# Kernel tuning notes

Measured on AMD Instinct MI355X. Metric: run time of the kernel, lower is better.

The kernel has to match this reference:

```python
import jax, jax.numpy as jnp
import numpy as np

NEG_SLOPE = 0.2  # both GATConv internal LeakyReLU and the module-level activation


def gat_conv(x, src, dst, W, a_src, a_dst, bias):
    """PyG GATConv (concat=True, add_self_loops handled by caller via src/dst).
    x: [N, Din]; W: [Din, H*C]; a_src, a_dst: [H, C]; bias: [H*C]."""
    N = x.shape[0]
    H, C = a_src.shape
    h = (x @ W).reshape(N, H, C)                       # [N, H, C]
    al_src = jnp.einsum('nhc,hc->nh', h, a_src)        # [N, H]
    al_dst = jnp.einsum('nhc,hc->nh', h, a_dst)        # [N, H]
    e = jax.nn.leaky_relu(al_src[src] + al_dst[dst], NEG_SLOPE)  # [E, H]
    # segment softmax over edges grouped by destination node
    m = jax.ops.segment_max(e, dst, num_segments=N)    # [N, H]
    ex = jnp.exp(e - m[dst])
    denom = jax.ops.segment_sum(ex, dst, num_segments=N)
    alpha = ex / denom[dst]                            # [E, H]
    out = jax.ops.segment_sum(alpha[:, :, None] * h[src], dst, num_segments=N)
    return out.reshape(N, H * C) + bias


def setup_inputs() -> dict:
    key = jax.random.key(0)
    N, E = 50000, 800000
    D_IN, HID, H = 128, 128, 2
    C = HID // H
    ks = jax.random.split(key, 20)
    inp = {
        'x': jax.random.normal(ks[0], (N, D_IN), dtype=jnp.float32),
        'edge_index': jax.random.randint(ks[1], (2, E), 0, N, dtype=jnp.int64),
    }
    dims = [D_IN, HID, HID]  # input dims of the 3 GATConv layers
    for i, din in enumerate(dims, start=1):
        s = 1.0 / np.sqrt(din)
        inp[f'W{i}'] = jax.random.normal(ks[2 + 4 * i], (din, HID), dtype=jnp.float32) * s
        inp[f'a_src{i}'] = jax.random.normal(ks[3 + 4 * i], (H, C), dtype=jnp.float32) * 0.1
        inp[f'a_dst{i}'] = jax.random.normal(ks[4 + 4 * i], (H, C), dtype=jnp.float32) * 0.1
        inp[f'b{i}'] = jnp.zeros((HID,), dtype=jnp.float32)
    inp['lin_w'] = jax.random.normal(ks[2], (HID, 1), dtype=jnp.float32) * (1.0 / np.sqrt(HID))
    inp['lin_b'] = jnp.zeros((1,), dtype=jnp.float32)
    return inp


def reference(x, edge_index, W1, a_src1, a_dst1, b1, W2, a_src2, a_dst2, b2,
              W3, a_src3, a_dst3, b3, lin_w, lin_b):
    N = x.shape[0]
    loops = jnp.arange(N, dtype=edge_index.dtype)
    src = jnp.concatenate([edge_index[0], loops])  # add_self_loops=True
    dst = jnp.concatenate([edge_index[1], loops])

    h = jax.nn.leaky_relu(gat_conv(x, src, dst, W1, a_src1, a_dst1, b1), NEG_SLOPE)
    # dropout is identity in eval mode (p=0.0)
    h = jax.nn.leaky_relu(h + gat_conv(h, src, dst, W2, a_src2, a_dst2, b2), NEG_SLOPE)
    h = jax.nn.leaky_relu(h + gat_conv(h, src, dst, W3, a_src3, a_dst3, b3), NEG_SLOPE)
    logits = (h @ lin_w + lin_b).squeeze(-1)  # [N]
    return logits
```

## Files before the change

kernel.cpp:

```cpp
#include <hip/hip_runtime.h>
#include <hip/hip_bf16.h>
#include <hip/hip_fp16.h>

#define LEAK 0.2f

typedef _Float16 half8  __attribute__((ext_vector_type(8)));
typedef _Float16 half4v __attribute__((ext_vector_type(4)));
typedef float    float4v __attribute__((ext_vector_type(4)));


__global__ __launch_bounds__(256) void k_bincount(const int* __restrict__ edst,
                                                  int* __restrict__ gbkt,
                                                  int E, int ETOT, int NBK) {
    __shared__ int lh[512];
    int t = threadIdx.x;
    for (int b = t; b < NBK; b += 256) lh[b] = 0;
    __syncthreads();
    int base = blockIdx.x * 4096;
    #pragma unroll
    for (int u = 0; u < 16; ++u) {
        int e = base + u * 256 + t;
        if (e < ETOT) {
            int d = (e < E) ? edst[e] : (e - E);
            atomicAdd(&lh[d >> 7], 1);
        }
    }
    __syncthreads();
    for (int b = t; b < NBK; b += 256)
        if (lh[b]) atomicAdd(&gbkt[b], lh[b]);
}

__global__ __launch_bounds__(512) void k_bktscan(const int* __restrict__ gbkt,
                                                 int* __restrict__ bko,
                                                 int* __restrict__ gcur, int NBK) {
    int t = threadIdx.x;
    int v = (t < NBK) ? gbkt[t] : 0;
    int lane = t & 63, wid = t >> 6;
    int x = v;
    #pragma unroll
    for (int o = 1; o < 64; o <<= 1) {
        int y = __shfl_up(x, o);
        if (lane >= o) x += y;
    }
    __shared__ int ws[8];
    if (lane == 63) ws[wid] = x;
    __syncthreads();
    if (wid == 0) {
        int s = (lane < 8) ? ws[lane] : 0;
        #pragma unroll
        for (int o = 1; o < 8; o <<= 1) {
            int y = __shfl_up(s, o);
            if (lane >= o) s += y;
        }
        if (lane < 8) ws[lane] = s;
    }
    __syncthreads();
    int excl = x - v + (wid > 0 ? ws[wid - 1] : 0);
    if (t < NBK) { bko[t] = excl; gcur[t] = excl; }
    if (t == 511) bko[NBK] = excl;
}

__global__ __launch_bounds__(256) void k_binscatter(const int* __restrict__ esrc,
                                                    const int* __restrict__ edst,
                                                    int* __restrict__ gcur,
                                                    unsigned int* __restrict__ binned,
                                                    int E, int ETOT, int NBK) {
    __shared__ int lh[512];
    __shared__ int lbase[512];
    int t = threadIdx.x;
    for (int b = t; b < NBK; b += 256) lh[b] = 0;
    __syncthreads();
    int base = blockIdx.x * 4096;
    unsigned int word[16]; int bb[16], rk[16];
    #pragma unroll
    for (int u = 0; u < 16; ++u) {
        int e = base + u * 256 + t;
        bb[u] = -1;
        if (e < ETOT) {
            int s, d;
            if (e < E) { s = esrc[e]; d = edst[e]; } else { s = d = e - E; }
            int b = d >> 7;
            bb[u] = b;
            rk[u] = atomicAdd(&lh[b], 1);
            word[u] = (unsigned int)s | ((unsigned int)(d & 127) << 17);
        }
    }
    __syncthreads();
    for (int b = t; b < NBK; b += 256) {
        int c = lh[b];
        lbase[b] = c ? atomicAdd(&gcur[b], c) : 0;
    }
    __syncthreads();
    #pragma unroll
    for (int u = 0; u < 16; ++u)
        if (bb[u] >= 0) binned[lbase[bb[u]] + rk[u]] = word[u];
}

__global__ __launch_bounds__(256) void k_scatter2(const unsigned int* __restrict__ binned,
                                                  const int* __restrict__ bko,
                                                  int* __restrict__ off,
                                                  int* __restrict__ csr, int N, int NBK) {
    __shared__ int deg[128];
    __shared__ int lcur[128];
    __shared__ int wt[2];
    int b = blockIdx.x, t = threadIdx.x;
    int n0 = b << 7;
    if (t < 128) deg[t] = 0;
    __syncthreads();
    int beg = bko[b], end = bko[b + 1];
    for (int i = beg + t; i < end; i += 256)
        atomicAdd(&deg[binned[i] >> 17], 1);
    __syncthreads();
    int v = 0, x = 0;
    if (t < 128) {
        v = deg[t];
        x = v;
        int lane = t & 63;
        #pragma unroll
        for (int o = 1; o < 64; o <<= 1) {
            int y = __shfl_up(x, o);
            if (lane >= o) x += y;
        }
        if (lane == 63) wt[t >> 6] = x;
    }
    __syncthreads();
    if (t < 128) {
        int excl = x - v + ((t >= 64) ? wt[0] : 0) + beg;
        lcur[t] = excl;
        int node = n0 + t;
        if (node < N) off[node] = excl;
    }
    if (b == NBK - 1 && t == 0) off[N] = end;
    __syncthreads();
    for (int i = beg + t; i < end; i += 256) {
        unsigned int u = binned[i];
        int pos = atomicAdd(&lcur[u >> 17], 1);
        csr[pos] = (int)(u & 0x1FFFF);
    }
}


__global__ __launch_bounds__(256) void k_wconv(const float* __restrict__ W0,
                                               const float* __restrict__ W1,
                                               const float* __restrict__ W2,
                                               _Float16* __restrict__ w16) {
    int i = blockIdx.x * 256 + threadIdx.x;
    if (i >= 3 * 16384) return;
    const float* src = (i < 16384) ? W0 : (i < 32768 ? W1 : W2);
    w16[i] = (_Float16)src[i & 16383];
}


__global__ __launch_bounds__(256) void k_gemm_mfma(const float* __restrict__ X,
                                                   const _Float16* __restrict__ Wh,
                                                   const float* __restrict__ a_src,
                                                   const float* __restrict__ a_dst,
                                                   __half* __restrict__ Hout,
                                                   float* __restrict__ alsrc,
                                                   float* __restrict__ aldst, int N) {
    __shared__ _Float16 As[64][136];
    __shared__ float sS[64][2];
    __shared__ float sD[64][2];
    const int t = threadIdx.x;
    const int lane = t & 63, w = t >> 6;
    const int block_row = blockIdx.x * 64;

    if (t < 128) { sS[t >> 1][t & 1] = 0.f; sD[t >> 1][t & 1] = 0.f; }

    #pragma unroll
    for (int it = 0; it < 8; ++it) {
        int i = t + 256 * it;
        int row = i >> 5, c4 = i & 31;
        int gr = block_row + row;
        float4 xv = make_float4(0.f, 0.f, 0.f, 0.f);
        if (gr < N) xv = *(const float4*)(X + (size_t)gr * 128 + c4 * 4);
        half4v hv;
        hv[0] = (_Float16)xv.x; hv[1] = (_Float16)xv.y;
        hv[2] = (_Float16)xv.z; hv[3] = (_Float16)xv.w;
        *(half4v*)(&As[row][c4 * 4]) = hv;
    }

    const int l15 = lane & 15, kq = (lane >> 4) * 8;
    half8 bf[2][4];
    #pragma unroll
    for (int ntl = 0; ntl < 2; ++ntl) {
        int n0 = (w * 2 + ntl) * 16 + l15;
        #pragma unroll
        for (int kt = 0; kt < 4; ++kt)
            #pragma unroll
            for (int j = 0; j < 8; ++j)
                bf[ntl][kt][j] = Wh[(kt * 32 + kq + j) * 128 + n0];
    }
    __syncthreads();

    float4v acc[4][2];
    #pragma unroll
    for (int mt = 0; mt < 4; ++mt)
        #pragma unroll
        for (int ntl = 0; ntl < 2; ++ntl)
            acc[mt][ntl] = (float4v){0.f, 0.f, 0.f, 0.f};

    #pragma unroll
    for (int kt = 0; kt < 4; ++kt) {
        half8 a[4];
        #pragma unroll
        for (int mt = 0; mt < 4; ++mt)
            a[mt] = *(const half8*)(&As[mt * 16 + l15][kt * 32 + kq]);
        #pragma unroll
        for (int mt = 0; mt < 4; ++mt)
            #pragma unroll
            for (int ntl = 0; ntl < 2; ++ntl)
                acc[mt][ntl] = __builtin_amdgcn_mfma_f32_16x16x32_f16(
                    a[mt], bf[ntl][kt], acc[mt][ntl], 0, 0, 0);
    }

    #pragma unroll
    for (int mt = 0; mt < 4; ++mt) {
        int r0 = block_row + mt * 16 + (lane >> 4) * 4;
        #pragma unroll
        for (int ntl = 0; ntl < 2; ++ntl) {
            int col = (w * 2 + ntl) * 16 + l15;
            #pragma unroll
            for (int reg = 0; reg < 4; ++reg) {
                int r = r0 + reg;
                if (r < N) Hout[(size_t)r * 128 + col] = __float2half((float)acc[mt][ntl][reg]);
            }
        }
    }

    {
        int c0 = w * 32 + l15, c1 = c0 + 16;
        float as0 = a_src[c0], as1 = a_src[c1];
        float ad0 = a_dst[c0], ad1 = a_dst[c1];
        int head = w >> 1;
        #pragma unroll
        for (int mt = 0; mt < 4; ++mt) {
            #pragma unroll
            for (int reg = 0; reg < 4; ++reg) {
                float ps = (float)acc[mt][0][reg] * as0 + (float)acc[mt][1][reg] * as1;
                float pd = (float)acc[mt][0][reg] * ad0 + (float)acc[mt][1][reg] * ad1;
                #pragma unroll
                for (int o = 1; o < 16; o <<= 1) {
                    ps += __shfl_xor(ps, o);
                    pd += __shfl_xor(pd, o);
                }
                if (l15 == 0) {
                    int row = mt * 16 + (lane >> 4) * 4 + reg;
                    atomicAdd(&sS[row][head], ps);
                    atomicAdd(&sD[row][head], pd);
                }
            }
        }
    }
    __syncthreads();
    if (t < 128) {
        int row = t >> 1, head = t & 1;
        int gr = block_row + row;
        if (gr < N) {
            alsrc[gr * 2 + head] = sS[row][head];
            aldst[gr * 2 + head] = sD[row][head];
        }
    }
}


__global__ __launch_bounds__(256) void k_aggregate(
        const __half* __restrict__ H16,
        const float* __restrict__ alsrc,
        const float* __restrict__ aldst,
        const int* __restrict__ off, const int* __restrict__ csr,
        const float* __restrict__ bias,
        const float* __restrict__ prev,
        float* __restrict__ Out,
        const float* __restrict__ lw, const float* __restrict__ lb,
        float* __restrict__ logits, int N, int mode) {
    int node = (int)((blockIdx.x * 256 + threadIdx.x) >> 6);
    int lane = threadIdx.x & 63;
    if (node >= N) return;
    int beg = off[node], end = off[node + 1];
    float ad0 = aldst[node * 2], ad1 = aldst[node * 2 + 1];

    int p = lane & 7;
    int q = lane >> 3;
    bool head0 = p < 4;
    const _Float16* hbase = (const _Float16*)H16 + p * 16;

    float acc[16];
    #pragma unroll
    for (int i = 0; i < 16; ++i) acc[i] = 0.f;
    float dsum = 0.f;

    for (int base = beg; base < end; base += 64) {
        int i = base + lane;
        float w0 = 0.f, w1 = 0.f; int s = 0;
        if (i < end) {
            s = csr[i];
            float2 al = *(const float2*)(&alsrc[s * 2]);
            float e0 = al.x + ad0; e0 = e0 > 0.f ? e0 : LEAK * e0;
            float e1 = al.y + ad1; e1 = e1 > 0.f ? e1 : LEAK * e1;
            w0 = __expf(e0); w1 = __expf(e1);
        }
        int cnt = min(64, end - base);
        int iters = (cnt + 7) >> 3;
        for (int jj = 0; jj < iters; ++jj) {
            int sl = (jj << 3) + q;
            int   sj  = __shfl(s,  sl);
            float w0j = __shfl(w0, sl);
            float w1j = __shfl(w1, sl);
            float wsel = head0 ? w0j : w1j;
            const _Float16* hp = hbase + (size_t)sj * 128;
            uint4 r0 = *(const uint4*)hp;
            uint4 r1 = *(const uint4*)(hp + 8);
            const _Float16* ha = (const _Float16*)&r0;
            const _Float16* hb = (const _Float16*)&r1;
            #pragma unroll
            for (int k = 0; k < 8; ++k) acc[k]     += wsel * (float)ha[k];
            #pragma unroll
            for (int k = 0; k < 8; ++k) acc[8 + k] += wsel * (float)hb[k];
            dsum += wsel;
        }
    }

    #pragma unroll
    for (int i = 0; i < 16; ++i) {
        acc[i] += __shfl_xor(acc[i], 8);
        acc[i] += __shfl_xor(acc[i], 16);
        acc[i] += __shfl_xor(acc[i], 32);
    }
    dsum += __shfl_xor(dsum, 8);
    dsum += __shfl_xor(dsum, 16);
    dsum += __shfl_xor(dsum, 32);

    if (q == 0) {
        float inv = 1.f / dsum;
        int c0 = p * 16;
        float v[16];
        #pragma unroll
        for (int i = 0; i < 16; ++i) v[i] = acc[i] * inv + bias[c0 + i];
        if (mode >= 1) {
            #pragma unroll
            for (int g = 0; g < 4; ++g) {
                float4 pv = *(const float4*)(&prev[(size_t)node * 128 + c0 + 4 * g]);
                v[4 * g]     += pv.x; v[4 * g + 1] += pv.y;
                v[4 * g + 2] += pv.z; v[4 * g + 3] += pv.w;
            }
        }
        #pragma unroll
        for (int i = 0; i < 16; ++i) v[i] = v[i] > 0.f ? v[i] : LEAK * v[i];
        if (mode == 2) {
            float partial = 0.f;
            #pragma unroll
            for (int i = 0; i < 16; ++i) partial += v[i] * lw[c0 + i];
            partial += __shfl_xor(partial, 1);
            partial += __shfl_xor(partial, 2);
            partial += __shfl_xor(partial, 4);
            if (p == 0) logits[node] = partial + lb[0];
        } else {
            #pragma unroll
            for (int g = 0; g < 4; ++g)
                *(float4*)(&Out[(size_t)node * 128 + c0 + 4 * g]) =
                    make_float4(v[4 * g], v[4 * g + 1], v[4 * g + 2], v[4 * g + 3]);
        }
    }
}


extern "C" void kernel_launch(void* const* d_in, const int* in_sizes, int n_in,
                              void* d_out, int out_size, void* d_ws, size_t ws_size,
                              hipStream_t stream) {
    const float* x    = (const float*)d_in[0];
    const int*   edge = (const int*)d_in[1];
    const float* W[3]  = {(const float*)d_in[2], (const float*)d_in[6], (const float*)d_in[10]};
    const float* as[3] = {(const float*)d_in[3], (const float*)d_in[7], (const float*)d_in[11]};
    const float* ad[3] = {(const float*)d_in[4], (const float*)d_in[8], (const float*)d_in[12]};
    const float* bs[3] = {(const float*)d_in[5], (const float*)d_in[9], (const float*)d_in[13]};
    const float* lw = (const float*)d_in[14];
    const float* lb = (const float*)d_in[15];

    const int N    = in_sizes[0] / 128;
    const int E    = in_sizes[1] / 2;
    const int ETOT = E + N;
    const int NBK  = (N + 127) >> 7;

    char* base = (char*)d_ws;
    size_t o = 0;
    auto carve = [&](size_t bytes) {
        char* p = base + o;
        o = (o + bytes + 255) & ~(size_t)255;
        return p;
    };
    int*      off    = (int*)     carve((size_t)(N + 1) * 4);
    int*      gbkt   = (int*)     carve((size_t)(NBK + 1) * 4);
    int*      bko    = (int*)     carve((size_t)(NBK + 1) * 4);
    int*      gcur   = (int*)     carve((size_t)(NBK + 1) * 4);
    unsigned* binned = (unsigned*)carve((size_t)ETOT * 4);
    int*      csr    = (int*)     carve((size_t)ETOT * 4);
    float*    alsrc  = (float*)   carve((size_t)N * 2 * 4);
    float*    aldst  = (float*)   carve((size_t)N * 2 * 4);
    __half*   h16    = (__half*)  carve((size_t)N * 128 * 2);
    float*    bufA   = (float*)   carve((size_t)N * 128 * 4);
    float*    bufB   = (float*)   carve((size_t)N * 128 * 4);
    _Float16* w16    = (_Float16*)carve((size_t)3 * 16384 * 2);
    (void)ws_size; (void)n_in; (void)out_size;

    const int* esrc = edge;
    const int* edst = edge + E;

    int eb = (ETOT + 4095) / 4096;

    hipMemsetAsync(gbkt, 0, (size_t)(NBK + 1) * 4, stream);
    k_wconv<<<192, 256, 0, stream>>>(W[0], W[1], W[2], w16);

    k_bincount<<<eb, 256, 0, stream>>>(edst, gbkt, E, ETOT, NBK);
    k_bktscan<<<1, 512, 0, stream>>>(gbkt, bko, gcur, NBK);
    k_binscatter<<<eb, 256, 0, stream>>>(esrc, edst, gcur, binned, E, ETOT, NBK);
    k_scatter2<<<NBK, 256, 0, stream>>>(binned, bko, off, csr, N, NBK);

    int gemm_blocks = (N + 63) / 64;
    int node_blocks = (N * 64 + 255) / 256;

    k_gemm_mfma<<<gemm_blocks, 256, 0, stream>>>(x, w16, as[0], ad[0], h16, alsrc, aldst, N);
    k_aggregate<<<node_blocks, 256, 0, stream>>>(h16, alsrc, aldst, off, csr,
                                                 bs[0], nullptr, bufA, lw, lb, nullptr, N, 0);
    k_gemm_mfma<<<gemm_blocks, 256, 0, stream>>>(bufA, w16 + 16384, as[1], ad[1], h16, alsrc, aldst, N);
    k_aggregate<<<node_blocks, 256, 0, stream>>>(h16, alsrc, aldst, off, csr,
                                                 bs[1], bufA, bufB, lw, lb, nullptr, N, 1);
    k_gemm_mfma<<<gemm_blocks, 256, 0, stream>>>(bufB, w16 + 32768, as[2], ad[2], h16, alsrc, aldst, N);
    k_aggregate<<<node_blocks, 256, 0, stream>>>(h16, alsrc, aldst, off, csr,
                                                 bs[2], bufB, nullptr, lw, lb, (float*)d_out, N, 2);
}
```

Baseline: 315.0 us.

## Slice feature matrix by column and split aggregation into alpha and gather kernels

The GEMM now writes projected features in a column-sliced layout: four slices of 32 halfs per node. Attention weights are computed and normalized once per edge by a new kernel and stored as (src, half2 alpha) pairs. A grid-strided gather kernel then reads each slice separately, so concurrent blocks hit a smaller feature working set, which is meant to improve cache locality for the random source gathers. The cost is an extra kernel launch per layer, an extra pass over edges that reads alsrc twice, fp16 rounding of alpha, and atomic adds for the final logits, which need a memset of the output.

```diff
diff --git a/kernel.cpp b/kernel.cpp
--- a/kernel.cpp
+++ b/kernel.cpp
@@ -155,7 +155,7 @@
                                                    const _Float16* __restrict__ Wh,
                                                    const float* __restrict__ a_src,
                                                    const float* __restrict__ a_dst,
-                                                   __half* __restrict__ Hout,
+                                                   _Float16* __restrict__ Hs,
                                                    float* __restrict__ alsrc,
                                                    float* __restrict__ aldst, int N) {
     __shared__ _Float16 As[64][136];
@@ -220,10 +220,12 @@
         #pragma unroll
         for (int ntl = 0; ntl < 2; ++ntl) {
             int col = (w * 2 + ntl) * 16 + l15;
+            int slice = col >> 5, cc = col & 31;
+            _Float16* dstp = Hs + ((size_t)slice * N) * 32 + cc;
             #pragma unroll
             for (int reg = 0; reg < 4; ++reg) {
                 int r = r0 + reg;
-                if (r < N) Hout[(size_t)r * 128 + col] = __float2half((float)acc[mt][ntl][reg]);
+                if (r < N) dstp[(size_t)r * 32] = (_Float16)acc[mt][ntl][reg];
             }
         }
     }
@@ -264,102 +266,140 @@
 }
 
 
-__global__ __launch_bounds__(256) void k_aggregate(
-        const __half* __restrict__ H16,
-        const float* __restrict__ alsrc,
-        const float* __restrict__ aldst,
-        const int* __restrict__ off, const int* __restrict__ csr,
+__global__ __launch_bounds__(256) void k_alphaw(const float* __restrict__ alsrc,
+                                                const float* __restrict__ aldst,
+                                                const int* __restrict__ off,
+                                                const int* __restrict__ csr,
+                                                int2* __restrict__ ewk, int N) {
+    int node = (int)((blockIdx.x * 256 + threadIdx.x) >> 6);
+    int lane = threadIdx.x & 63;
+    if (node >= N) return;
+    int beg = off[node], end = off[node + 1];
+    float ad0 = aldst[node * 2], ad1 = aldst[node * 2 + 1];
+
+    int i0 = beg + lane;
+    int s0 = 0; float w0 = 0.f, w1 = 0.f;
+    if (i0 < end) {
+        s0 = csr[i0];
+        float2 al = *(const float2*)(&alsrc[s0 * 2]);
+        float e0 = al.x + ad0; e0 = e0 > 0.f ? e0 : LEAK * e0;
+        float e1 = al.y + ad1; e1 = e1 > 0.f ? e1 : LEAK * e1;
+        w0 = __expf(e0); w1 = __expf(e1);
+    }
+    float d0 = w0, d1 = w1;
+    for (int base2 = beg + 64; base2 < end; base2 += 64) {
+        int i = base2 + lane;
+        if (i < end) {
+            int s = csr[i];
+            float2 al = *(const float2*)(&alsrc[s * 2]);
+            float e0 = al.x + ad0; e0 = e0 > 0.f ? e0 : LEAK * e0;
+            float e1 = al.y + ad1; e1 = e1 > 0.f ? e1 : LEAK * e1;
+            d0 += __expf(e0); d1 += __expf(e1);
+        }
+    }
+    #pragma unroll
+    for (int o = 1; o < 64; o <<= 1) { d0 += __shfl_xor(d0, o); d1 += __shfl_xor(d1, o); }
+    float inv0 = 1.f / d0, inv1 = 1.f / d1;
+
+    if (i0 < end) {
+        union { __half2 h; int i; } u;
+        u.h = __halves2half2(__float2half_rn(w0 * inv0), __float2half_rn(w1 * inv1));
+        ewk[i0] = make_int2(s0, u.i);
+    }
+    for (int base2 = beg + 64; base2 < end; base2 += 64) {
+        int i = base2 + lane;
+        if (i < end) {
+            int s = csr[i];
+            float2 al = *(const float2*)(&alsrc[s * 2]);
+            float e0 = al.x + ad0; e0 = e0 > 0.f ? e0 : LEAK * e0;
+            float e1 = al.y + ad1; e1 = e1 > 0.f ? e1 : LEAK * e1;
+            union { __half2 h; int i; } u;
+            u.h = __halves2half2(__float2half_rn(__expf(e0) * inv0),
+                                 __float2half_rn(__expf(e1) * inv1));
+            ewk[i] = make_int2(s, u.i);
+        }
+    }
+}
+
+
+__global__ __launch_bounds__(256) void k_gather(
+        const _Float16* __restrict__ Hs,
+        const int2* __restrict__ ewk,
+        const int* __restrict__ off,
         const float* __restrict__ bias,
         const float* __restrict__ prev,
         float* __restrict__ Out,
         const float* __restrict__ lw, const float* __restrict__ lb,
         float* __restrict__ logits, int N, int mode) {
-    int node = (int)((blockIdx.x * 256 + threadIdx.x) >> 6);
+    int b = blockIdx.x;
+    int slice = (b & 7) >> 1;
+    int widx = (b >> 3) * 2 + (b & 1);
+    int wave0 = widx * 4 + (threadIdx.x >> 6);
+    int nW = (gridDim.x >> 3) * 8;
     int lane = threadIdx.x & 63;
-    if (node >= N) return;
-    int beg = off[node], end = off[node + 1];
-    float ad0 = aldst[node * 2], ad1 = aldst[node * 2 + 1];
-
-    int p = lane & 7;
-    int q = lane >> 3;
-    bool head0 = p < 4;
-    const _Float16* hbase = (const _Float16*)H16 + p * 16;
-
-    float acc[16];
-    #pragma unroll
-    for (int i = 0; i < 16; ++i) acc[i] = 0.f;
-    float dsum = 0.f;
-
-    for (int base = beg; base < end; base += 64) {
-        int i = base + lane;
-        float w0 = 0.f, w1 = 0.f; int s = 0;
-        if (i < end) {
-            s = csr[i];
-            float2 al = *(const float2*)(&alsrc[s * 2]);
-            float e0 = al.x + ad0; e0 = e0 > 0.f ? e0 : LEAK * e0;
-            float e1 = al.y + ad1; e1 = e1 > 0.f ? e1 : LEAK * e1;
-            w0 = __expf(e0); w1 = __expf(e1);
-        }
-        int cnt = min(64, end - base);
-        int iters = (cnt + 7) >> 3;
-        for (int jj = 0; jj < iters; ++jj) {
-            int sl = (jj << 3) + q;
-            int   sj  = __shfl(s,  sl);
-            float w0j = __shfl(w0, sl);
-            float w1j = __shfl(w1, sl);
-            float wsel = head0 ? w0j : w1j;
-            const _Float16* hp = hbase + (size_t)sj * 128;
-            uint4 r0 = *(const uint4*)hp;
-            uint4 r1 = *(const uint4*)(hp + 8);
-            const _Float16* ha = (const _Float16*)&r0;
-            const _Float16* hb = (const _Float16*)&r1;
-            #pragma unroll
-            for (int k = 0; k < 8; ++k) acc[k]     += wsel * (float)ha[k];
-            #pragma unroll
-            for (int k = 0; k < 8; ++k) acc[8 + k] += wsel * (float)hb[k];
-            dsum += wsel;
-        }
-    }
-
-    #pragma unroll
-    for (int i = 0; i < 16; ++i) {
-        acc[i] += __shfl_xor(acc[i], 8);
-        acc[i] += __shfl_xor(acc[i], 16);
-        acc[i] += __shfl_xor(acc[i], 32);
-    }
-    dsum += __shfl_xor(dsum, 8);
-    dsum += __shfl_xor(dsum, 16);
-    dsum += __shfl_xor(dsum, 32);
-
-    if (q == 0) {
-        float inv = 1.f / dsum;
-        int c0 = p * 16;
-        float v[16];
-        #pragma unroll
-        for (int i = 0; i < 16; ++i) v[i] = acc[i] * inv + bias[c0 + i];
-        if (mode >= 1) {
-            #pragma unroll
-            for (int g = 0; g < 4; ++g) {
-                float4 pv = *(const float4*)(&prev[(size_t)node * 128 + c0 + 4 * g]);
-                v[4 * g]     += pv.x; v[4 * g + 1] += pv.y;
-                v[4 * g + 2] += pv.z; v[4 * g + 3] += pv.w;
+    int p = lane & 3, q = lane >> 2;
+    const _Float16* hbase = Hs + (size_t)slice * N * 32 + p * 8;
+    bool head0 = slice < 2;
+    int cbase = slice * 32 + p * 8;
+
+    for (int node = wave0; node < N; node += nW) {
+        int beg = off[node], end = off[node + 1];
+        float acc[8];
+        #pragma unroll
+        for (int k = 0; k < 8; ++k) acc[k] = 0.f;
+
+        for (int base2 = beg; base2 < end; base2 += 64) {
+            int i = base2 + lane;
+            int sv = 0, av = 0;
+            if (i < end) { int2 e = ewk[i]; sv = e.x; av = e.y; }
+            int cnt = min(64, end - base2);
+            int iters = (cnt + 15) >> 4;
+            for (int jj = 0; jj < iters; ++jj) {
+                int sl = (jj << 4) + q;
+                int sj = __shfl(sv, sl);
+                int aj = __shfl(av, sl);
+                __half2 ah = *(__half2*)&aj;
+                float asel = head0 ? __low2float(ah) : __high2float(ah);
+                const _Float16* hp = hbase + (size_t)sj * 32;
+                uint4 raw = *(const uint4*)hp;
+                const _Float16* h = (const _Float16*)&raw;
+                #pragma unroll
+                for (int k = 0; k < 8; ++k) acc[k] += asel * (float)h[k];
             }
         }
-        #pragma unroll
-        for (int i = 0; i < 16; ++i) v[i] = v[i] > 0.f ? v[i] : LEAK * v[i];
-        if (mode == 2) {
-            float partial = 0.f;
-            #pragma unroll
-            for (int i = 0; i < 16; ++i) partial += v[i] * lw[c0 + i];
-            partial += __shfl_xor(partial, 1);
-            partial += __shfl_xor(partial, 2);
-            partial += __shfl_xor(partial, 4);
-            if (p == 0) logits[node] = partial + lb[0];
-        } else {
-            #pragma unroll
-            for (int g = 0; g < 4; ++g)
-                *(float4*)(&Out[(size_t)node * 128 + c0 + 4 * g]) =
-                    make_float4(v[4 * g], v[4 * g + 1], v[4 * g + 2], v[4 * g + 3]);
+
+        #pragma unroll
+        for (int k = 0; k < 8; ++k) {
+            acc[k] += __shfl_xor(acc[k], 4);
+            acc[k] += __shfl_xor(acc[k], 8);
+            acc[k] += __shfl_xor(acc[k], 16);
+            acc[k] += __shfl_xor(acc[k], 32);
+        }
+
+        if (q == 0) {
+            float v[8];
+            #pragma unroll
+            for (int k = 0; k < 8; ++k) v[k] = acc[k] + bias[cbase + k];
+            if (mode >= 1) {
+                float4 p0 = *(const float4*)(&prev[(size_t)node * 128 + cbase]);
+                float4 p1 = *(const float4*)(&prev[(size_t)node * 128 + cbase + 4]);
+                v[0] += p0.x; v[1] += p0.y; v[2] += p0.z; v[3] += p0.w;
+                v[4] += p1.x; v[5] += p1.y; v[6] += p1.z; v[7] += p1.w;
+            }
+            #pragma unroll
+            for (int k = 0; k < 8; ++k) v[k] = v[k] > 0.f ? v[k] : LEAK * v[k];
+            if (mode == 2) {
+                float partial = 0.f;
+                #pragma unroll
+                for (int k = 0; k < 8; ++k) partial += v[k] * lw[cbase + k];
+                partial += __shfl_xor(partial, 1);
+                partial += __shfl_xor(partial, 2);
+                if (p == 0)
+                    atomicAdd(&logits[node], partial + (slice == 0 ? lb[0] : 0.f));
+            } else {
+                *(float4*)(&Out[(size_t)node * 128 + cbase])     = make_float4(v[0], v[1], v[2], v[3]);
+                *(float4*)(&Out[(size_t)node * 128 + cbase + 4]) = make_float4(v[4], v[5], v[6], v[7]);
+            }
         }
     }
 }
@@ -395,9 +435,10 @@
     int*      gcur   = (int*)     carve((size_t)(NBK + 1) * 4);
     unsigned* binned = (unsigned*)carve((size_t)ETOT * 4);
     int*      csr    = (int*)     carve((size_t)ETOT * 4);
+    int2*     ewk    = (int2*)    carve((size_t)ETOT * 8);
     float*    alsrc  = (float*)   carve((size_t)N * 2 * 4);
     float*    aldst  = (float*)   carve((size_t)N * 2 * 4);
-    __half*   h16    = (__half*)  carve((size_t)N * 128 * 2);
+    _Float16* h16    = (_Float16*)carve((size_t)N * 128 * 2);
     float*    bufA   = (float*)   carve((size_t)N * 128 * 4);
     float*    bufB   = (float*)   carve((size_t)N * 128 * 4);
     _Float16* w16    = (_Float16*)carve((size_t)3 * 16384 * 2);
@@ -409,6 +450,7 @@
     int eb = (ETOT + 4095) / 4096;
 
     hipMemsetAsync(gbkt, 0, (size_t)(NBK + 1) * 4, stream);
+    hipMemsetAsync(d_out, 0, (size_t)N * 4, stream);
     k_wconv<<<192, 256, 0, stream>>>(W[0], W[1], W[2], w16);
 
     k_bincount<<<eb, 256, 0, stream>>>(edst, gbkt, E, ETOT, NBK);
@@ -418,14 +460,18 @@
 
     int gemm_blocks = (N + 63) / 64;
     int node_blocks = (N * 64 + 255) / 256;
+    int gather_blocks = 8192;
 
     k_gemm_mfma<<<gemm_blocks, 256, 0, stream>>>(x, w16, as[0], ad[0], h16, alsrc, aldst, N);
-    k_aggregate<<<node_blocks, 256, 0, stream>>>(h16, alsrc, aldst, off, csr,
-                                                 bs[0], nullptr, bufA, lw, lb, nullptr, N, 0);
+    k_alphaw<<<node_blocks, 256, 0, stream>>>(alsrc, aldst, off, csr, ewk, N);
+    k_gather<<<gather_blocks, 256, 0, stream>>>(h16, ewk, off, bs[0], nullptr, bufA,
+                                                lw, lb, nullptr, N, 0);
     k_gemm_mfma<<<gemm_blocks, 256, 0, stream>>>(bufA, w16 + 16384, as[1], ad[1], h16, alsrc, aldst, N);
-    k_aggregate<<<node_blocks, 256, 0, stream>>>(h16, alsrc, aldst, off, csr,
-                                                 bs[1], bufA, bufB, lw, lb, nullptr, N, 1);
+    k_alphaw<<<node_blocks, 256, 0, stream>>>(alsrc, aldst, off, csr, ewk, N);
+    k_gather<<<gather_blocks, 256, 0, stream>>>(h16, ewk, off, bs[1], bufA, bufB,
+                                                lw, lb, nullptr, N, 1);
     k_gemm_mfma<<<gemm_blocks, 256, 0, stream>>>(bufB, w16 + 32768, as[2], ad[2], h16, alsrc, aldst, N);
-    k_aggregate<<<node_blocks, 256, 0, stream>>>(h16, alsrc, aldst, off, csr,
-                                                 bs[2], bufB, nullptr, lw, lb, (float*)d_out, N, 2);
-}
+    k_alphaw<<<node_blocks, 256, 0, stream>>>(alsrc, aldst, off, csr, ewk, N);
+    k_gather<<<gather_blocks, 256, 0, stream>>>(h16, ewk, off, bs[2], bufB, nullptr,
+                                                lw, lb, (float*)d_out, N, 2);
+}
```

New measurement: 485.8 us. +54.2%, slower.
